# Kernel tuning notes

Measured on AMD Instinct MI355X. Metric: run time of the kernel, lower is better.

Reference implementation:

```python
import jax, jax.numpy as jnp
import numpy as np

D_MODEL = 1024
N_HEADS = 16
HEAD_DIM = 64
T = 4096
ROT = HEAD_DIM // 2          # 32 channels get rotary
PAIR = ROT // 2              # 16 cos/sin frequencies
EPS = 1e-6
SCALE = 0.12                 # constant attention scale (not 1/sqrt(d))
ROPE_BASE = 10000.0
VOCAB = 50257


def setup_inputs() -> dict:
    key = jax.random.key(0)
    k_x, k_qkv, k_o, k_tok = jax.random.split(key, 4)
    bound = 0.5 / np.sqrt(D_MODEL)
    x = jax.random.normal(k_x, (1, T, D_MODEL), dtype=jnp.float32)
    w_qkv = jax.random.uniform(k_qkv, (3 * D_MODEL, D_MODEL), jnp.float32, -bound, bound)
    # module uses zero_init for w_o; use small random so output is non-trivial
    w_o = jax.random.uniform(k_o, (D_MODEL, D_MODEL), jnp.float32, -bound, bound)
    q_norm_w = jnp.ones((HEAD_DIM,), jnp.float32)
    k_norm_w = jnp.ones((HEAD_DIM,), jnp.float32)
    tokens = jax.random.randint(k_tok, (1, T), 0, VOCAB, dtype=jnp.int64)
    pos = jnp.arange(T, dtype=jnp.int64)
    # RotaryCache: inv_freq over pair dims, cos/sin of t * inv_freq
    inv_freq = 1.0 / (ROPE_BASE ** (jnp.arange(PAIR, dtype=jnp.float32) / PAIR))
    freqs = jnp.arange(T, dtype=jnp.float32)[:, None] * inv_freq[None, :]  # [T, PAIR]
    return {
        "x": x, "tokens": tokens, "pos": pos,
        "w_qkv": w_qkv, "w_o": w_o,
        "q_norm_w": q_norm_w, "k_norm_w": k_norm_w,
        "cos": jnp.cos(freqs), "sin": jnp.sin(freqs),
        "window_tokens": 1024, "block_size": 128,
    }


def _rmsnorm(x, w):
    var = jnp.mean(x * x, axis=-1, keepdims=True)
    return x * jax.lax.rsqrt(var + EPS) * w


def reference(x, tokens, pos, w_qkv, w_o, q_norm_w, k_norm_w, cos, sin,
              window_tokens, block_size):
    B, Tq, C = x.shape
    H, Dh = N_HEADS, HEAD_DIM
    qkv = x @ w_qkv.T                                  # [B, T, 3C]
    q, k, v = jnp.split(qkv, 3, axis=-1)

    def to_bhtd(t):
        return t.reshape(B, Tq, H, Dh).transpose(0, 2, 1, 3)
    q, k, v = to_bhtd(q), to_bhtd(k), to_bhtd(v)

    q = _rmsnorm(q, q_norm_w)
    k = _rmsnorm(k, k_norm_w)

    # half-truncated RoPE: rotate first ROT channels pairwise (even/odd)
    c = cos[pos][None, None]                           # [1,1,T,PAIR]
    s = sin[pos][None, None]

    def rope_rotate(t):
        t1, t2 = t[..., :ROT], t[..., ROT:]
        even, odd = t1[..., 0::2], t1[..., 1::2]
        r_even = even * c - odd * s
        r_odd = even * s + odd * c
        t1r = jnp.stack([r_even, r_odd], axis=-1).reshape(t1.shape)
        return jnp.concatenate([t1r, t2], axis=-1)

    q = rope_rotate(q)
    k = rope_rotate(k)

    v = v * 0.5                                        # no value-embed branch

    scores = jnp.einsum('bhtd,bhsd->bhts', q, k) * SCALE
    idx = jnp.arange(Tq)
    diff = idx[:, None] - idx[None, :]
    allowed = (diff >= 0) & (diff < window_tokens)     # sliding causal window
    scores = jnp.where(allowed, scores, -jnp.inf)
    p = jax.nn.softmax(scores, axis=-1)
    out = jnp.einsum('bhts,bhsd->bhtd', p, v)
    out = out.transpose(0, 2, 1, 3).reshape(B, Tq, C)
    return out @ w_o.T
```

## Files before the change

### kernel.cpp

```cpp
#include <hip/hip_runtime.h>


typedef __bf16 bf16x8 __attribute__((ext_vector_type(8)));
typedef __bf16 bf16x2 __attribute__((ext_vector_type(2)));
typedef float f32x4 __attribute__((ext_vector_type(4)));
typedef unsigned short u16x8 __attribute__((ext_vector_type(8)));
typedef unsigned short u16x4 __attribute__((ext_vector_type(4)));

#define MFMA16(a, b, c) __builtin_amdgcn_mfma_f32_16x16x32_bf16((a), (b), (c), 0, 0, 0)

__device__ __forceinline__ unsigned short f2bf(float f) {
    unsigned int u = __float_as_uint(f);
    u += 0x7fffu + ((u >> 16) & 1u);
    return (unsigned short)(u >> 16);
}
__device__ __forceinline__ float bf2f(unsigned short h) {
    return __uint_as_float(((unsigned int)h) << 16);
}
__device__ __forceinline__ unsigned int pk2bf(float a, float b) {
#if __has_builtin(__builtin_amdgcn_cvt_pk_bf16_f32)
    bf16x2 v = __builtin_amdgcn_cvt_pk_bf16_f32(a, b);
    return __builtin_bit_cast(unsigned int, v);
#else
    return (unsigned int)f2bf(a) | ((unsigned int)f2bf(b) << 16);
#endif
}
__device__ __forceinline__ float fexp2(float x) {
#if __has_builtin(__builtin_amdgcn_exp2f)
    return __builtin_amdgcn_exp2f(x);
#else
    return exp2f(x);
#endif
}

__device__ __forceinline__ void gl_lds16(const void* g, void* l) {
    typedef __attribute__((address_space(1))) unsigned int GU;
    typedef __attribute__((address_space(3))) unsigned int LU;
    __builtin_amdgcn_global_load_lds((GU*)(unsigned long long)g,
                                     (LU*)(unsigned int)(unsigned long long)l,
                                     16, 0, 0);
}

__global__ void cvt3_kernel(const float* __restrict__ x,
                            const float* __restrict__ wqkv,
                            const float* __restrict__ wo,
                            unsigned short* __restrict__ xb,
                            unsigned short* __restrict__ wqkvb,
                            unsigned short* __restrict__ wob) {
    int i = blockIdx.x * 256 + threadIdx.x;
    const float* src;
    unsigned short* dst;
    int off;
    if (i < 1048576) { src = x; dst = xb; off = i; }
    else if (i < 1835008) { src = wqkv; dst = wqkvb; off = i - 1048576; }
    else { src = wo; dst = wob; off = i - 1835008; }
    float4 f = ((const float4*)src)[off];
    u16x4 o;
    o[0] = f2bf(f.x); o[1] = f2bf(f.y); o[2] = f2bf(f.z); o[3] = f2bf(f.w);
    ((u16x4*)dst)[off] = o;
}

#define TBS 72
__global__ __launch_bounds__(256, 6) void gemm_qkv(
    const unsigned short* __restrict__ A,
    const unsigned short* __restrict__ Bt,
    const float* __restrict__ cosb, const float* __restrict__ sinb,
    const float* __restrict__ qw, const float* __restrict__ kw,
    unsigned short* __restrict__ Qb,
    unsigned short* __restrict__ Kb,
    unsigned short* __restrict__ Vt)
{
    __shared__ unsigned short As[64 * 32];
    __shared__ unsigned short Bs[128 * 32];
    __shared__ unsigned short tb[4][16 * TBS];
    const int tid = threadIdx.x;
    const int wave = tid >> 6, lane = tid & 63;
    const int quad = lane >> 4, l16 = lane & 15;
    const int m0 = blockIdx.x * 64, n0 = blockIdx.y * 128;
    const int wm = (wave >> 1) * 32, wn = (wave & 1) * 64;

    f32x4 acc[2][4];
#pragma unroll
    for (int i = 0; i < 2; ++i)
#pragma unroll
        for (int j = 0; j < 4; ++j) acc[i][j] = (f32x4){0.f, 0.f, 0.f, 0.f};

    for (int k0 = 0; k0 < 1024; k0 += 32) {
        {
            const int e = (wave * 64 + lane) * 8;
            const int r = e >> 5, col = e & 31;
            gl_lds16(A + (size_t)(m0 + r) * 1024 + (k0 + col), &As[wave * 512]);
        }
#pragma unroll
        for (int i = 0; i < 2; ++i) {
            const int c = wave * 2 + i;
            const int e = (c * 64 + lane) * 8;
            const int r = e >> 5, col = e & 31;
            gl_lds16(Bt + (size_t)(n0 + r) * 1024 + (k0 + col), &Bs[c * 512]);
        }
        __syncthreads();
        bf16x8 af[2], bfr[4];
#pragma unroll
        for (int mt = 0; mt < 2; ++mt)
            af[mt] = *(const bf16x8*)&As[(wm + mt * 16 + l16) * 32 + quad * 8];
#pragma unroll
        for (int nt = 0; nt < 4; ++nt)
            bfr[nt] = *(const bf16x8*)&Bs[(wn + nt * 16 + l16) * 32 + quad * 8];
#pragma unroll
        for (int mt = 0; mt < 2; ++mt)
#pragma unroll
            for (int nt = 0; nt < 4; ++nt)
                acc[mt][nt] = MFMA16(af[mt], bfr[nt], acc[mt][nt]);
        __syncthreads();
    }

    const int region = blockIdx.y >> 3;
    const int h = ((blockIdx.y & 7) << 1) + (wave & 1);
    unsigned short* tbw = tb[wave];

    if (region < 2) {
        const float* wgt = region ? kw : qw;
        unsigned short* dst = region ? Kb : Qb;
        const float post = region ? 1.f : 0.17312340490667046f;
        float w[4];
#pragma unroll
        for (int nt = 0; nt < 4; ++nt) w[nt] = wgt[nt * 16 + l16] * post;
#pragma unroll
        for (int mt = 0; mt < 2; ++mt) {
#pragma unroll
            for (int r = 0; r < 4; ++r) {
                const int row = m0 + wm + mt * 16 + quad * 4 + r;
                float ss = 0.f;
#pragma unroll
                for (int nt = 0; nt < 4; ++nt)
                    ss += acc[mt][nt][r] * acc[mt][nt][r];
                ss += __shfl_xor(ss, 1); ss += __shfl_xor(ss, 2);
                ss += __shfl_xor(ss, 4); ss += __shfl_xor(ss, 8);
                const float rn = rsqrtf(ss * (1.f / 64.f) + 1e-6f);
                float val[4];
#pragma unroll
                for (int nt = 0; nt < 4; ++nt)
                    val[nt] = acc[mt][nt][r] * rn * w[nt];
#pragma unroll
                for (int nt = 0; nt < 2; ++nt) {
                    const float prt = __shfl_xor(val[nt], 1);
                    const int p = nt * 8 + (l16 >> 1);
                    const float c = cosb[row * 16 + p];
                    const float s = sinb[row * 16 + p];
                    val[nt] = (l16 & 1) ? (prt * s + val[nt] * c)
                                        : (val[nt] * c - prt * s);
                }
#pragma unroll
                for (int nt = 0; nt < 4; ++nt)
                    tbw[(quad * 4 + r) * TBS + nt * 16 + l16] = f2bf(val[nt]);
            }
            const int t = lane >> 2, dcol = (lane & 3) * 16;
            u16x8 v0 = *(const u16x8*)&tbw[t * TBS + dcol];
            u16x8 v1 = *(const u16x8*)&tbw[t * TBS + dcol + 8];
            const size_t ob = ((size_t)h * 4096 + (m0 + wm + mt * 16 + t)) * 64 + dcol;
            *(u16x8*)&dst[ob] = v0;
            *(u16x8*)&dst[ob + 8] = v1;
        }
    } else {
#pragma unroll
        for (int mt = 0; mt < 2; ++mt) {
#pragma unroll
            for (int nt = 0; nt < 4; ++nt)
#pragma unroll
                for (int r = 0; r < 4; ++r)
                    tbw[(nt * 16 + l16) * 16 + quad * 4 + r] =
                        f2bf(acc[mt][nt][r] * 0.5f);
            u16x8 v0 = *(const u16x8*)&tbw[lane * 16];
            u16x8 v1 = *(const u16x8*)&tbw[lane * 16 + 8];
            const size_t vo = ((size_t)h * 64 + lane) * 4096 + m0 + wm + mt * 16;
            *(u16x8*)&Vt[vo] = v0;
            *(u16x8*)&Vt[vo + 8] = v1;
        }
    }
}

#define PSTR 72

template <int MODE>
__device__ __forceinline__ void attn_step(
    int s0, int tq, int wave, int quad, int l16, int krow, int kcol,
    const unsigned short* __restrict__ Kh, const unsigned short* __restrict__ Vh,
    unsigned short* Ks0, unsigned short* Ks1,
    unsigned short* Vs0, unsigned short* Vs1, unsigned short* Pw,
    const bf16x8 qf0, const bf16x8 qf1, f32x4 (&o)[4], float& lsum)
{
    __syncthreads();
    const unsigned short* kb = Kh + (size_t)(s0 + krow) * 64 + kcol;
    const unsigned short* vb = Vh + (size_t)krow * 4096 + s0 + kcol;
    gl_lds16(kb,      &Ks0[wave * 512]);
    gl_lds16(kb + 32, &Ks1[wave * 512]);
    gl_lds16(vb,      &Vs0[wave * 512]);
    gl_lds16(vb + 32, &Vs1[wave * 512]);
    __syncthreads();

#pragma unroll
    for (int i = 0; i < 4; ++i) {
        const bf16x8 kf0 = *(const bf16x8*)&Ks0[(i * 16 + l16) * 32 + quad * 8];
        const bf16x8 kf1 = *(const bf16x8*)&Ks1[(i * 16 + l16) * 32 + quad * 8];
        f32x4 z = (f32x4){0.f, 0.f, 0.f, 0.f};
        z = MFMA16(kf0, qf0, z);
        z = MFMA16(kf1, qf1, z);
        float p[4];
#pragma unroll
        for (int r = 0; r < 4; ++r) {
            float e = fexp2(z[r]);
            if (MODE == 1) {
                const int s = s0 + i * 16 + quad * 4 + r;
                e = ((tq - s) < 1024) ? e : 0.f;
            }
            if (MODE == 2) {
                const int s = s0 + i * 16 + quad * 4 + r;
                e = (s <= tq) ? e : 0.f;
            }
            p[r] = e;
            lsum += e;
        }
        uint2 pk;
        pk.x = pk2bf(p[0], p[1]);
        pk.y = pk2bf(p[2], p[3]);
        *(uint2*)&Pw[l16 * PSTR + i * 16 + quad * 4] = pk;
    }
    const bf16x8 pf0 = *(const bf16x8*)&Pw[l16 * PSTR + quad * 8];
    const bf16x8 pf1 = *(const bf16x8*)&Pw[l16 * PSTR + 32 + quad * 8];
#pragma unroll
    for (int dt = 0; dt < 4; ++dt) {
        const bf16x8 vf0 = *(const bf16x8*)&Vs0[(dt * 16 + l16) * 32 + quad * 8];
        const bf16x8 vf1 = *(const bf16x8*)&Vs1[(dt * 16 + l16) * 32 + quad * 8];
        o[dt] = MFMA16(pf0, vf0, o[dt]);
        o[dt] = MFMA16(pf1, vf1, o[dt]);
    }
}

__global__ __launch_bounds__(256) void attn_kernel(
    const unsigned short* __restrict__ Qb,
    const unsigned short* __restrict__ Kb,
    const unsigned short* __restrict__ Vt,
    unsigned short* __restrict__ att)
{
    __shared__ unsigned short Ks0[64 * 32];
    __shared__ unsigned short Ks1[64 * 32];
    __shared__ unsigned short Vs0[64 * 32];
    __shared__ unsigned short Vs1[64 * 32];
    __shared__ unsigned short P[4][16 * PSTR];

    const int bid = blockIdx.x;
    const int h = ((bid & 7) << 1) | ((bid >> 3) & 1);
    const int t0 = (63 - (bid >> 4)) * 64;

    const int tid = threadIdx.x;
    const int wave = tid >> 6, lane = tid & 63;
    const int quad = lane >> 4, l16 = lane & 15;
    const int qt0 = t0 + wave * 16;
    const int tq = qt0 + l16;
    const int krow = tid >> 2, kcol = (tid & 3) * 8;

    const unsigned short* Qh = Qb + (size_t)h * 4096 * 64;
    const unsigned short* Kh = Kb + (size_t)h * 4096 * 64;
    const unsigned short* Vh = Vt + (size_t)h * 64 * 4096;

    const bf16x8 qf0 = *(const bf16x8*)&Qh[(qt0 + l16) * 64 + quad * 8];
    const bf16x8 qf1 = *(const bf16x8*)&Qh[(qt0 + l16) * 64 + 32 + quad * 8];

    f32x4 o[4];
#pragma unroll
    for (int dt = 0; dt < 4; ++dt) o[dt] = (f32x4){0.f, 0.f, 0.f, 0.f};
    float lsum = 0.f;
    unsigned short* Pw = P[wave];

    int s0 = (t0 >= 1024) ? (t0 - 1024) : 0;
    if (t0 >= 1024) {
        attn_step<1>(s0, tq, wave, quad, l16, krow, kcol, Kh, Vh,
                     Ks0, Ks1, Vs0, Vs1, Pw, qf0, qf1, o, lsum);
        s0 += 64;
    }
    for (; s0 < t0; s0 += 64)
        attn_step<0>(s0, tq, wave, quad, l16, krow, kcol, Kh, Vh,
                     Ks0, Ks1, Vs0, Vs1, Pw, qf0, qf1, o, lsum);
    attn_step<2>(t0, tq, wave, quad, l16, krow, kcol, Kh, Vh,
                 Ks0, Ks1, Vs0, Vs1, Pw, qf0, qf1, o, lsum);

    lsum += __shfl_xor(lsum, 16);
    lsum += __shfl_xor(lsum, 32);
    float lr[4];
#pragma unroll
    for (int r = 0; r < 4; ++r) lr[r] = 1.f / __shfl(lsum, quad * 4 + r);
#pragma unroll
    for (int dt = 0; dt < 4; ++dt)
#pragma unroll
        for (int r = 0; r < 4; ++r)
            att[(size_t)(qt0 + quad * 4 + r) * 1024 + h * 64 + dt * 16 + l16] =
                f2bf(o[dt][r] * lr[r]);
}

template <int BM, bool F32OUT>
__global__ __launch_bounds__(256) void gemm_bt(
    const unsigned short* __restrict__ A,
    const unsigned short* __restrict__ Bt,
    void* __restrict__ Cp, int N, int K) {
    __shared__ unsigned short As[BM * 32];
    __shared__ unsigned short Bs[128 * 32];
    constexpr int MT = BM / 32;
    const int tid = threadIdx.x;
    const int wave = tid >> 6, lane = tid & 63;
    const int quad = lane >> 4, l16 = lane & 15;
    const int m0 = blockIdx.x * BM, n0 = blockIdx.y * 128;
    const int wm = (wave >> 1) * (BM / 2), wn = (wave & 1) * 64;

    f32x4 acc[MT][4];
#pragma unroll
    for (int i = 0; i < MT; ++i)
#pragma unroll
        for (int j = 0; j < 4; ++j) acc[i][j] = (f32x4){0.f, 0.f, 0.f, 0.f};

    for (int k0 = 0; k0 < K; k0 += 32) {
#pragma unroll
        for (int i = 0; i < BM / 64; ++i) {
            const int c = wave * (BM / 64) + i;
            const int e = (c * 64 + lane) * 8;
            const int r = e >> 5, col = e & 31;
            gl_lds16(A + (size_t)(m0 + r) * K + (k0 + col), &As[c * 512]);
        }
#pragma unroll
        for (int i = 0; i < 2; ++i) {
            const int c = wave * 2 + i;
            const int e = (c * 64 + lane) * 8;
            const int r = e >> 5, col = e & 31;
            gl_lds16(Bt + (size_t)(n0 + r) * K + (k0 + col), &Bs[c * 512]);
        }
        __syncthreads();
        bf16x8 af[MT], bfr[4];
#pragma unroll
        for (int mt = 0; mt < MT; ++mt)
            af[mt] = *(const bf16x8*)&As[(wm + mt * 16 + l16) * 32 + quad * 8];
#pragma unroll
        for (int nt = 0; nt < 4; ++nt)
            bfr[nt] = *(const bf16x8*)&Bs[(wn + nt * 16 + l16) * 32 + quad * 8];
#pragma unroll
        for (int mt = 0; mt < MT; ++mt)
#pragma unroll
            for (int nt = 0; nt < 4; ++nt)
                acc[mt][nt] = MFMA16(af[mt], bfr[nt], acc[mt][nt]);
        __syncthreads();
    }
#pragma unroll
    for (int mt = 0; mt < MT; ++mt)
#pragma unroll
        for (int nt = 0; nt < 4; ++nt)
#pragma unroll
            for (int r = 0; r < 4; ++r) {
                const int row = m0 + wm + mt * 16 + quad * 4 + r;
                const int col = n0 + wn + nt * 16 + l16;
                const float v = acc[mt][nt][r];
                if (F32OUT)
                    ((float*)Cp)[(size_t)row * N + col] = v;
                else
                    ((unsigned short*)Cp)[(size_t)row * N + col] = f2bf(v);
            }
}

extern "C" void kernel_launch(void* const* d_in, const int* in_sizes, int n_in,
                              void* d_out, int out_size, void* d_ws, size_t ws_size,
                              hipStream_t stream) {
    const float* x    = (const float*)d_in[0];
    const float* wqkv = (const float*)d_in[3];
    const float* wo   = (const float*)d_in[4];
    const float* qw   = (const float*)d_in[5];
    const float* kw   = (const float*)d_in[6];
    const float* cosb = (const float*)d_in[7];
    const float* sinb = (const float*)d_in[8];

    char* ws = (char*)d_ws;
    if (ws_size < (size_t)48 * 1024 * 1024) return;
    unsigned short* xb    = (unsigned short*)(ws + ((size_t)0 << 20));
    unsigned short* wqkvb = (unsigned short*)(ws + ((size_t)8 << 20));
    unsigned short* wob   = (unsigned short*)(ws + ((size_t)14 << 20));
    unsigned short* Qb    = (unsigned short*)(ws + ((size_t)16 << 20));
    unsigned short* Kb    = (unsigned short*)(ws + ((size_t)24 << 20));
    unsigned short* Vt    = (unsigned short*)(ws + ((size_t)32 << 20));
    unsigned short* attb  = (unsigned short*)(ws + ((size_t)40 << 20));

    cvt3_kernel<<<8192, 256, 0, stream>>>(x, wqkv, wo, xb, wqkvb, wob);

    gemm_qkv<<<dim3(64, 24), 256, 0, stream>>>(xb, wqkvb, cosb, sinb, qw, kw,
                                               Qb, Kb, Vt);

    attn_kernel<<<1024, 256, 0, stream>>>(Qb, Kb, Vt, attb);

    gemm_bt<64, true><<<dim3(64, 8), 256, 0, stream>>>(attb, wob, (float*)d_out, 1024, 1024);
}
```

Baseline: 197.4 us.

## Double-buffer LDS in output GEMM and widen K-step in QKV GEMM

The QKV GEMM now loads a 64-wide K slice per iteration into two LDS halves, which halves the number of barriers per K loop. It reuses one shared buffer for both the tile staging and the epilogue transpose scratch. The generic gemm_bt kernel gains ping-pong LDS buffers so that the next K tile's global-to-LDS loads are issued before the current tile's MFMAs, overlapping memory with compute. The cost is more LDS per block, which may reduce occupancy. The single barrier per iteration in the double-buffered loop also relies on the async-load wait semantics being correct.

```diff
diff --git a/kernel.cpp b/kernel.cpp
--- a/kernel.cpp
+++ b/kernel.cpp
@@ -70,9 +70,12 @@
     unsigned short* __restrict__ Kb,
     unsigned short* __restrict__ Vt)
 {
-    __shared__ unsigned short As[64 * 32];
-    __shared__ unsigned short Bs[128 * 32];
-    __shared__ unsigned short tb[4][16 * TBS];
+    __shared__ unsigned short smem[12288];
+    unsigned short* As0 = smem;
+    unsigned short* As1 = smem + 2048;
+    unsigned short* Bs0 = smem + 4096;
+    unsigned short* Bs1 = smem + 8192;
+
     const int tid = threadIdx.x;
     const int wave = tid >> 6, lane = tid & 63;
     const int quad = lane >> 4, l16 = lane & 15;
@@ -85,38 +88,56 @@
 #pragma unroll
         for (int j = 0; j < 4; ++j) acc[i][j] = (f32x4){0.f, 0.f, 0.f, 0.f};
 
-    for (int k0 = 0; k0 < 1024; k0 += 32) {
+    const int lrow = lane >> 2, lcol = (lane & 3) * 8;
+
+    for (int k0 = 0; k0 < 1024; k0 += 64) {
         {
-            const int e = (wave * 64 + lane) * 8;
-            const int r = e >> 5, col = e & 31;
-            gl_lds16(A + (size_t)(m0 + r) * 1024 + (k0 + col), &As[wave * 512]);
+            const unsigned short* ab = A + (size_t)(m0 + wave * 16 + lrow) * 1024 + k0 + lcol;
+            gl_lds16(ab,      &As0[wave * 512]);
+            gl_lds16(ab + 32, &As1[wave * 512]);
         }
 #pragma unroll
         for (int i = 0; i < 2; ++i) {
             const int c = wave * 2 + i;
-            const int e = (c * 64 + lane) * 8;
-            const int r = e >> 5, col = e & 31;
-            gl_lds16(Bt + (size_t)(n0 + r) * 1024 + (k0 + col), &Bs[c * 512]);
+            const unsigned short* bb = Bt + (size_t)(n0 + c * 16 + lrow) * 1024 + k0 + lcol;
+            gl_lds16(bb,      &Bs0[c * 512]);
+            gl_lds16(bb + 32, &Bs1[c * 512]);
         }
         __syncthreads();
-        bf16x8 af[2], bfr[4];
-#pragma unroll
-        for (int mt = 0; mt < 2; ++mt)
-            af[mt] = *(const bf16x8*)&As[(wm + mt * 16 + l16) * 32 + quad * 8];
-#pragma unroll
-        for (int nt = 0; nt < 4; ++nt)
-            bfr[nt] = *(const bf16x8*)&Bs[(wn + nt * 16 + l16) * 32 + quad * 8];
-#pragma unroll
-        for (int mt = 0; mt < 2; ++mt)
+        {
+            bf16x8 af[2], bfr[4];
+#pragma unroll
+            for (int mt = 0; mt < 2; ++mt)
+                af[mt] = *(const bf16x8*)&As0[(wm + mt * 16 + l16) * 32 + quad * 8];
 #pragma unroll
             for (int nt = 0; nt < 4; ++nt)
-                acc[mt][nt] = MFMA16(af[mt], bfr[nt], acc[mt][nt]);
+                bfr[nt] = *(const bf16x8*)&Bs0[(wn + nt * 16 + l16) * 32 + quad * 8];
+#pragma unroll
+            for (int mt = 0; mt < 2; ++mt)
+#pragma unroll
+                for (int nt = 0; nt < 4; ++nt)
+                    acc[mt][nt] = MFMA16(af[mt], bfr[nt], acc[mt][nt]);
+        }
+        {
+            bf16x8 af[2], bfr[4];
+#pragma unroll
+            for (int mt = 0; mt < 2; ++mt)
+                af[mt] = *(const bf16x8*)&As1[(wm + mt * 16 + l16) * 32 + quad * 8];
+#pragma unroll
+            for (int nt = 0; nt < 4; ++nt)
+                bfr[nt] = *(const bf16x8*)&Bs1[(wn + nt * 16 + l16) * 32 + quad * 8];
+#pragma unroll
+            for (int mt = 0; mt < 2; ++mt)
+#pragma unroll
+                for (int nt = 0; nt < 4; ++nt)
+                    acc[mt][nt] = MFMA16(af[mt], bfr[nt], acc[mt][nt]);
+        }
         __syncthreads();
     }
 
+    unsigned short* tbw = smem + wave * 1152;
     const int region = blockIdx.y >> 3;
     const int h = ((blockIdx.y & 7) << 1) + (wave & 1);
-    unsigned short* tbw = tb[wave];
 
     if (region < 2) {
         const float* wgt = region ? kw : qw;
@@ -302,8 +323,8 @@
     const unsigned short* __restrict__ A,
     const unsigned short* __restrict__ Bt,
     void* __restrict__ Cp, int N, int K) {
-    __shared__ unsigned short As[BM * 32];
-    __shared__ unsigned short Bs[128 * 32];
+    __shared__ unsigned short As[2][BM * 32];
+    __shared__ unsigned short Bs[2][128 * 32];
     constexpr int MT = BM / 32;
     const int tid = threadIdx.x;
     const int wave = tid >> 6, lane = tid & 63;
@@ -317,35 +338,42 @@
 #pragma unroll
         for (int j = 0; j < 4; ++j) acc[i][j] = (f32x4){0.f, 0.f, 0.f, 0.f};
 
-    for (int k0 = 0; k0 < K; k0 += 32) {
+    auto stageAB = [&](int buf, int k0) {
 #pragma unroll
         for (int i = 0; i < BM / 64; ++i) {
             const int c = wave * (BM / 64) + i;
             const int e = (c * 64 + lane) * 8;
             const int r = e >> 5, col = e & 31;
-            gl_lds16(A + (size_t)(m0 + r) * K + (k0 + col), &As[c * 512]);
+            gl_lds16(A + (size_t)(m0 + r) * K + (k0 + col), &As[buf][c * 512]);
         }
 #pragma unroll
         for (int i = 0; i < 2; ++i) {
             const int c = wave * 2 + i;
             const int e = (c * 64 + lane) * 8;
             const int r = e >> 5, col = e & 31;
-            gl_lds16(Bt + (size_t)(n0 + r) * K + (k0 + col), &Bs[c * 512]);
-        }
-        __syncthreads();
+            gl_lds16(Bt + (size_t)(n0 + r) * K + (k0 + col), &Bs[buf][c * 512]);
+        }
+    };
+
+    stageAB(0, 0);
+    __syncthreads();
+    int buf = 0;
+    for (int k0 = 0; k0 < K; k0 += 32) {
+        if (k0 + 32 < K) stageAB(buf ^ 1, k0 + 32);
         bf16x8 af[MT], bfr[4];
 #pragma unroll
         for (int mt = 0; mt < MT; ++mt)
-            af[mt] = *(const bf16x8*)&As[(wm + mt * 16 + l16) * 32 + quad * 8];
+            af[mt] = *(const bf16x8*)&As[buf][(wm + mt * 16 + l16) * 32 + quad * 8];
 #pragma unroll
         for (int nt = 0; nt < 4; ++nt)
-            bfr[nt] = *(const bf16x8*)&Bs[(wn + nt * 16 + l16) * 32 + quad * 8];
+            bfr[nt] = *(const bf16x8*)&Bs[buf][(wn + nt * 16 + l16) * 32 + quad * 8];
 #pragma unroll
         for (int mt = 0; mt < MT; ++mt)
 #pragma unroll
             for (int nt = 0; nt < 4; ++nt)
                 acc[mt][nt] = MFMA16(af[mt], bfr[nt], acc[mt][nt]);
         __syncthreads();
+        buf ^= 1;
     }
 #pragma unroll
     for (int mt = 0; mt < MT; ++mt)
```

Result: faster. 188.0 us (-4.8%).
